# Kernel tuning notes

Measured on AMD Instinct MI355X. Metric: run time of the kernel, lower is better.

Reference implementation:

```python
import jax, jax.numpy as jnp
import numpy as np

M = 2048                      # image side (self.M)
INPUT_SHAPE = (362, 362)      # default forward arg; only used for pad sizing
N_ANGLES = 32
THETA = np.linspace(0.0, np.pi, N_ANGLES)  # radians, as the source uses np.cos(angle)


def _dct_mat(N):
    # DCT-II with norm='ortho': C[k, n] = s_k * cos(pi*(n+0.5)*k/N)
    n = np.arange(N)
    C = np.cos(np.pi * (n[None, :] + 0.5) * n[:, None] / N)
    scale = np.full((N, 1), np.sqrt(2.0 / N))
    scale[0, 0] = np.sqrt(1.0 / N)
    return jnp.asarray((C * scale).astype(np.float32))


def _pad_width():
    diagonal = np.sqrt(2) * max(INPUT_SHAPE)
    pad = [int(np.ceil(diagonal - s)) for s in INPUT_SHAPE]
    new_center = [(s + p) // 2 for s, p in zip(INPUT_SHAPE, pad)]
    old_center = [s // 2 for s in INPUT_SHAPE]
    pad_before = [nc - oc for oc, nc in zip(old_center, new_center)]
    return [(pb, p - pb) for pb, p in zip(pad_before, pad)]


def setup_inputs() -> dict:
    key = jax.random.key(0)
    image = jax.random.normal(key, (M, M), dtype=jnp.float32)
    return {"image": image}


def _forward(image):
    # --- 2D DCT-II (ortho), separable: D = C @ x @ C^T ---
    C = _dct_mat(M)
    d = C @ image @ C.T

    # --- pad (widths derived from input_shape as in the source) ---
    padded = jnp.pad(d, _pad_width())          # [P, P], P = 2198
    P = padded.shape[0]
    center = P // 2

    xs = jnp.arange(P, dtype=jnp.float32)
    yy, xx = jnp.meshgrid(xs, xs, indexing='ij')   # output row (y) / col (x) grid
    angles = jnp.asarray(THETA, dtype=jnp.float32)

    def one_angle(carry, ang):
        cos_a = jnp.cos(ang)
        sin_a = jnp.sin(ang)
        # ImageProjectiveTransformV3 maps output (x, y) -> input coords
        x_in = cos_a * xx + sin_a * yy - center * (cos_a + sin_a - 1.0)
        y_in = -sin_a * xx + cos_a * yy - center * (cos_a - sin_a - 1.0)
        x0 = jnp.floor(x_in)
        y0 = jnp.floor(y_in)
        wx = x_in - x0
        wy = y_in - y0
        # fill_mode='WRAP': wrap sample coordinates modulo image size
        x0i = jnp.mod(x0.astype(jnp.int32), P)
        x1i = (x0i + 1) % P
        y0i = jnp.mod(y0.astype(jnp.int32), P)
        y1i = (y0i + 1) % P
        v00 = padded[y0i, x0i]
        v01 = padded[y0i, x1i]
        v10 = padded[y1i, x0i]
        v11 = padded[y1i, x1i]
        rotated = (1.0 - wy) * ((1.0 - wx) * v00 + wx * v01) \
                + wy * ((1.0 - wx) * v10 + wx * v11)
        # radon line: reduce over rows (axis=0)
        return carry, rotated.sum(axis=0)

    _, lines = jax.lax.scan(one_angle, 0, angles)   # [A, P]
    y = lines.T                                     # [P, A] == tf.transpose(A)
    return y / jnp.max(y)


def reference(image):
    return _forward(image)
```

## Files before the change

kernel.cpp:

```cpp
#include <hip/hip_runtime.h>
#include <hip/hip_bf16.h>
#include <math.h>

#define PDIM 2198
#define PDIM2 2252
#define PADB 75
#define NANG 32
#define NLINE (NANG * PDIM)

#define CB 32
#define RW 32
#define NWIN 69
#define TS 48
#define TSTRIDE 52
#define NBUF 4

typedef __attribute__((ext_vector_type(8))) short bf16x8;
typedef __attribute__((ext_vector_type(4))) float f32x4;

#define GLOAD_LDS16(g, l)                                              \
    __builtin_amdgcn_global_load_lds(                                  \
        (const __attribute__((address_space(1))) void*)(g),            \
        (__attribute__((address_space(3))) void*)(l), 16, 0, 0)

#if __has_builtin(__builtin_amdgcn_fractf)
#define FRACTF(x) __builtin_amdgcn_fractf(x)
#else
#define FRACTF(x) ((x) - floorf(x))
#endif

__global__ void gen_dct(__hip_bfloat16* __restrict__ C) {
    int idx = blockIdx.x * 256 + threadIdx.x;
    int k = idx >> 11;
    int n = idx & 2047;
    int t = ((2 * n + 1) * k) & 8191;
    float s = sqrtf(((k == 0) ? 1.0f : 2.0f) / 2048.0f);
    C[idx] = __float2bfloat16(s * cospif((float)t * (1.0f / 4096.0f)));
}

__global__ void cvt_img(const float* __restrict__ in, __hip_bfloat16* __restrict__ out) {
    int i = (blockIdx.x * 256 + threadIdx.x) * 4;
    float4 v = *(const float4*)(in + i);
    out[i + 0] = __float2bfloat16(v.x);
    out[i + 1] = __float2bfloat16(v.y);
    out[i + 2] = __float2bfloat16(v.z);
    out[i + 3] = __float2bfloat16(v.w);
}

template<int F32OUT>
__global__ __launch_bounds__(256) void gemm_bt(const __hip_bfloat16* __restrict__ A,
                                               const __hip_bfloat16* __restrict__ B,
                                               void* __restrict__ out,
                                               int ldo, int off) {
    __shared__ __hip_bfloat16 Al[128 * 32];
    __shared__ __hip_bfloat16 Bl[64 * 32];
    const int tid = threadIdx.x;
    const int wid = tid >> 6;
    const int lane = tid & 63;
    const int wr = wid >> 1, wc = wid & 1;
    const int l15 = lane & 15, lhi = lane >> 4;
    const int row0 = blockIdx.y * 128;
    const int col0 = blockIdx.x * 64;

    const __hip_bfloat16* gA = A + (size_t)(row0 + wid * 32 + (lane >> 2)) * 2048 + (lane & 3) * 8;
    const __hip_bfloat16* gB = B + (size_t)(col0 + wid * 16 + (lane >> 2)) * 2048 + (lane & 3) * 8;
    __hip_bfloat16* lA = Al + wid * 1024;
    __hip_bfloat16* lB = Bl + wid * 512;

    f32x4 acc[4][2] = {};

    for (int k0 = 0; k0 < 2048; k0 += 32) {
        GLOAD_LDS16(gA + k0, lA);
        GLOAD_LDS16(gA + 16 * 2048 + k0, lA + 16 * 32);
        GLOAD_LDS16(gB + k0, lB);
        __syncthreads();
        bf16x8 af[4], bfr[2];
#pragma unroll
        for (int m = 0; m < 4; ++m)
            af[m] = *(const bf16x8*)(Al + (wr * 64 + m * 16 + l15) * 32 + lhi * 8);
#pragma unroll
        for (int n = 0; n < 2; ++n)
            bfr[n] = *(const bf16x8*)(Bl + (wc * 32 + n * 16 + l15) * 32 + lhi * 8);
#pragma unroll
        for (int m = 0; m < 4; ++m)
#pragma unroll
            for (int n = 0; n < 2; ++n)
                acc[m][n] = __builtin_amdgcn_mfma_f32_16x16x32_bf16(af[m], bfr[n],
                                                                    acc[m][n], 0, 0, 0);
        __syncthreads();
    }

#pragma unroll
    for (int m = 0; m < 4; ++m) {
        const int row = row0 + wr * 64 + m * 16 + lhi * 4;
#pragma unroll
        for (int n = 0; n < 2; ++n) {
            const int col = col0 + wc * 32 + n * 16 + l15;
            f32x4 v = acc[m][n];
            if (F32OUT) {
                float* p = (float*)out + (size_t)(col + off) * ldo + off + row;
                p[0] = v[0]; p[1] = v[1]; p[2] = v[2]; p[3] = v[3];
            } else {
                __hip_bfloat16* p = (__hip_bfloat16*)out + (size_t)col * 2048 + row;
                p[0] = __float2bfloat16(v[0]);
                p[1] = __float2bfloat16(v[1]);
                p[2] = __float2bfloat16(v[2]);
                p[3] = __float2bfloat16(v[3]);
            }
        }
    }
}

struct AngleArgs {
    float ca[NANG], sa[NANG], ox[NANG], oy[NANG];
};

__global__ __launch_bounds__(256) void radon6(const float* __restrict__ padded,
                                              float* __restrict__ lines,
                                              AngleArgs args) {
    __shared__ float tile[NBUF][TS * TSTRIDE];
    __shared__ float red[4][8];
    const int a = blockIdx.y;
    const int c0 = blockIdx.x * CB;
    const int t = threadIdx.x;
    const int wid = t >> 6, lane = t & 63;
    const int cl = lane >> 3;
    const int rl = lane & 7;
    const int c = c0 + wid * 8 + cl;
    const float ca = args.ca[a], sa = args.sa[a];
    const float ox = args.ox[a], oy = args.oy[a];

    const float cf = (float)c;
    const float xbase = fmaf(ca, cf, ox);
    const float ybase = fmaf(-sa, cf, oy);

    const float xbMin = fminf(fmaf(ca, (float)c0, ox), fmaf(ca, (float)(c0 + CB - 1), ox));
    const float ybMin = fminf(fmaf(-sa, (float)c0, oy), fmaf(-sa, (float)(c0 + CB - 1), oy));
    const bool caPos = (ca >= 0.0f);

    float sum = 0.0f;

    auto origin = [&](int w, int& bx0, int& by0) {
        const float rx = (float)(w * RW);
        const float ry = caPos ? rx : (float)(w * RW + RW - 1);
        bx0 = (int)floorf(fmaf(sa, rx, xbMin)) - 1;
        by0 = (int)floorf(fmaf(ca, ry, ybMin)) - 1;
    };

    auto stage = [&](int buf, int bx0, int by0) {
        int bxs = bx0;
        bxs += (bxs < 0) ? PDIM : 0;
        bxs -= (bxs >= PDIM) ? PDIM : 0;
        const int slab = wid * 12;
#pragma unroll
        for (int iss = 0; iss < 3; ++iss) {
            const int d = iss * 256 + lane * 4;
            if (d < 12 * TSTRIDE) {
                const int rr = d / TSTRIDE;
                const int col = d - rr * TSTRIDE;
                int gy = by0 + slab + rr;
                gy += (gy < 0) ? PDIM : 0;
                gy -= (gy >= PDIM) ? PDIM : 0;
                GLOAD_LDS16(padded + (size_t)gy * PDIM2 + bxs + col,
                            &tile[buf][slab * TSTRIDE + iss * 256]);
            }
        }
    };

    auto compute = [&](int r0, int buf, int bx0, int by0, bool last) {
        const float xbb = xbase - (float)bx0;
        const float ybb = ybase - (float)by0;
        const float* tb = &tile[buf][0];
#pragma unroll
        for (int k = 0; k < 4; ++k) {
            const int r = r0 + rl + 8 * k;
            const float rf = (float)r;
            const float xl = fmaf(sa, rf, xbb);
            const float yl = fmaf(ca, rf, ybb);
            const int xi = (int)xl;
            const int yi = (int)yl;
            const float wx = FRACTF(xl);
            const float wy = FRACTF(yl);
            const float* p = tb + yi * TSTRIDE + xi;
            const float v00 = p[0], v01 = p[1];
            const float v10 = p[TSTRIDE], v11 = p[TSTRIDE + 1];
            const float top = fmaf(wx, v01 - v00, v00);
            const float bot = fmaf(wx, v11 - v10, v10);
            if (!last || r < PDIM) sum = fmaf(wy, bot - top, sum + top);
        }
    };

    int bx[NWIN > 0 ? 4 : 4], by[4];
    origin(0, bx[0], by[0]);
    stage(0, bx[0], by[0]);
    origin(1, bx[1], by[1]);
    stage(1, bx[1], by[1]);
    for (int w = 0; w < NWIN; ++w) {
        if (w + 2 < NWIN) {
            int bxn, byn;
            origin(w + 2, bxn, byn);
            bx[(w + 2) & 3] = bxn; by[(w + 2) & 3] = byn;
            stage((w + 2) & 3, bxn, byn);
        }
        if (w < NWIN - 2)       asm volatile("s_waitcnt vmcnt(6)" ::: "memory");
        else if (w == NWIN - 2) asm volatile("s_waitcnt vmcnt(3)" ::: "memory");
        else                    asm volatile("s_waitcnt vmcnt(0)" ::: "memory");
        __builtin_amdgcn_s_barrier();
        __builtin_amdgcn_sched_barrier(0);
        compute(w * RW, w & 3, bx[w & 3], by[w & 3], w == NWIN - 1);
    }

    sum += __shfl_xor(sum, 1, 64);
    sum += __shfl_xor(sum, 2, 64);
    sum += __shfl_xor(sum, 4, 64);
    if (rl == 0) red[wid][cl] = sum;
    __syncthreads();
    if (t < 32 && c0 + t < PDIM)
        lines[a * PDIM + c0 + t] = red[t >> 3][t & 7];
}

__global__ __launch_bounds__(256) void max_k(const float* __restrict__ lines,
                                             unsigned int* __restrict__ gmax) {
    const int idx = blockIdx.x * 256 + threadIdx.x;
    float m = (idx < NLINE) ? lines[idx] : -3.4e38f;
#pragma unroll
    for (int off = 32; off > 0; off >>= 1)
        m = fmaxf(m, __shfl_down(m, off, 64));
    __shared__ float wm[4];
    const int lane = threadIdx.x & 63, wid = threadIdx.x >> 6;
    if (lane == 0) wm[wid] = m;
    __syncthreads();
    if (threadIdx.x == 0) {
        float bm = fmaxf(fmaxf(wm[0], wm[1]), fmaxf(wm[2], wm[3]));
        unsigned int b = __float_as_uint(bm);
        unsigned int key = (b & 0x80000000u) ? ~b : (b | 0x80000000u);
        atomicMax(gmax, key);
    }
}

__global__ void norm_k(const float* __restrict__ lines,
                       const unsigned int* __restrict__ gmax,
                       float* __restrict__ out) {
    int idx = blockIdx.x * 256 + threadIdx.x;
    if (idx >= NLINE) return;
    unsigned int u = *gmax;
    unsigned int b = (u & 0x80000000u) ? (u & 0x7fffffffu) : ~u;
    float mx = __uint_as_float(b);
    int c = idx >> 5;
    int a = idx & 31;
    out[idx] = lines[(size_t)a * PDIM + c] / mx;
}

extern "C" void kernel_launch(void* const* d_in, const int* in_sizes, int n_in,
                              void* d_out, int out_size, void* d_ws, size_t ws_size,
                              hipStream_t stream) {
    (void)in_sizes; (void)n_in; (void)out_size; (void)ws_size;
    const float* img = (const float*)d_in[0];
    float* out = (float*)d_out;

    __hip_bfloat16* Cbf   = (__hip_bfloat16*)d_ws;
    __hip_bfloat16* imgbf = Cbf + 4194304;
    __hip_bfloat16* uT    = imgbf + 4194304;
    float* padded  = (float*)(uT + 4194304);
    float* lines   = padded + (size_t)PDIM * PDIM2;
    unsigned int* gmax = (unsigned int*)(lines + NLINE);

    hipMemsetAsync(padded, 0, (size_t)PDIM * PDIM2 * sizeof(float), stream);
    hipMemsetAsync(gmax, 0, sizeof(unsigned int), stream);

    gen_dct<<<16384, 256, 0, stream>>>(Cbf);
    cvt_img<<<4096, 256, 0, stream>>>(img, imgbf);

    gemm_bt<0><<<dim3(32, 16), 256, 0, stream>>>(imgbf, Cbf, uT, 2048, 0);
    gemm_bt<1><<<dim3(32, 16), 256, 0, stream>>>(uT, Cbf, padded, PDIM2, PADB);

    AngleArgs aa;
    for (int i = 0; i < NANG; ++i) {
        float th = (float)((double)i * 3.14159265358979323846 / 31.0);
        float ca = (float)cos((double)th);
        float sa = (float)sin((double)th);
        aa.ca[i] = ca;
        aa.sa[i] = sa;
        aa.ox[i] = -1099.0f * (ca + sa - 1.0f);
        aa.oy[i] = -1099.0f * (ca - sa - 1.0f);
    }
    radon6<<<dim3(NWIN, NANG), 256, 0, stream>>>(padded, lines, aa);
    max_k<<<(NLINE + 255) / 256, 256, 0, stream>>>(lines, gmax);
    norm_k<<<(NLINE + 255) / 256, 256, 0, stream>>>(lines, gmax, out);
}
```

Measured before the change: 318.8 us.

## Zero only pad borders and use triple-buffered radon staging

Replaces the full memset of the padded buffer with a kernel that zeroes only the pad border rows and columns, since the GEMM writes the interior. This avoids rewriting roughly 20 MB of memory. The radon kernel moves from four LDS buffers to three, issues each prefetch after the barrier, and specializes the last-window bounds check at compile time. Fewer buffers cut LDS use and could raise occupancy, but the prefetch is now issued later, which may expose more load latency.

```diff
diff --git a/kernel.cpp b/kernel.cpp
--- a/kernel.cpp
+++ b/kernel.cpp
@@ -13,10 +13,12 @@
 #define NWIN 69
 #define TS 48
 #define TSTRIDE 52
-#define NBUF 4
+#define NBUF 3
 
 typedef __attribute__((ext_vector_type(8))) short bf16x8;
 typedef __attribute__((ext_vector_type(4))) float f32x4;
+
+template<bool L> struct BoolC { static constexpr bool value = L; };
 
 #define GLOAD_LDS16(g, l)                                              \
     __builtin_amdgcn_global_load_lds(                                  \
@@ -45,6 +47,24 @@
     out[i + 1] = __float2bfloat16(v.y);
     out[i + 2] = __float2bfloat16(v.z);
     out[i + 3] = __float2bfloat16(v.w);
+}
+
+__global__ __launch_bounds__(256) void pad_zero(float* __restrict__ padded) {
+    int idx = blockIdx.x * 256 + threadIdx.x;
+    const int TOPBOT = 2 * PADB * PDIM2;
+    if (idx < TOPBOT) {
+        int r = idx / PDIM2;
+        int c = idx - r * PDIM2;
+        int row = (r < PADB) ? r : (2048 + r);
+        padded[(size_t)row * PDIM2 + c] = 0.0f;
+    } else {
+        int i2 = idx - TOPBOT;
+        if (i2 >= 2048 * 204) return;
+        int rr = i2 / 204;
+        int s = i2 - rr * 204;
+        int col = (s < PADB) ? s : (2048 + s);
+        padded[(size_t)(PADB + rr) * PDIM2 + col] = 0.0f;
+    }
 }
 
 template<int F32OUT>
@@ -115,7 +135,7 @@
     float ca[NANG], sa[NANG], ox[NANG], oy[NANG];
 };
 
-__global__ __launch_bounds__(256) void radon6(const float* __restrict__ padded,
+__global__ __launch_bounds__(256) void radon7(const float* __restrict__ padded,
                                               float* __restrict__ lines,
                                               AngleArgs args) {
     __shared__ float tile[NBUF][TS * TSTRIDE];
@@ -167,7 +187,7 @@
         }
     };
 
-    auto compute = [&](int r0, int buf, int bx0, int by0, bool last) {
+    auto computeT = [&](int r0, int buf, int bx0, int by0, auto lastc) {
         const float xbb = xbase - (float)bx0;
         const float ybb = ybase - (float)by0;
         const float* tb = &tile[buf][0];
@@ -186,28 +206,28 @@
             const float v10 = p[TSTRIDE], v11 = p[TSTRIDE + 1];
             const float top = fmaf(wx, v01 - v00, v00);
             const float bot = fmaf(wx, v11 - v10, v10);
-            if (!last || r < PDIM) sum = fmaf(wy, bot - top, sum + top);
+            if (!decltype(lastc)::value || r < PDIM) sum = fmaf(wy, bot - top, sum + top);
         }
     };
 
-    int bx[NWIN > 0 ? 4 : 4], by[4];
-    origin(0, bx[0], by[0]);
-    stage(0, bx[0], by[0]);
-    origin(1, bx[1], by[1]);
-    stage(1, bx[1], by[1]);
+    int bxr[3], byr[3];
+    origin(0, bxr[0], byr[0]);
+    stage(0, bxr[0], byr[0]);
+    origin(1, bxr[1], byr[1]);
+    stage(1, bxr[1], byr[1]);
     for (int w = 0; w < NWIN; ++w) {
-        if (w + 2 < NWIN) {
-            int bxn, byn;
-            origin(w + 2, bxn, byn);
-            bx[(w + 2) & 3] = bxn; by[(w + 2) & 3] = byn;
-            stage((w + 2) & 3, bxn, byn);
-        }
-        if (w < NWIN - 2)       asm volatile("s_waitcnt vmcnt(6)" ::: "memory");
-        else if (w == NWIN - 2) asm volatile("s_waitcnt vmcnt(3)" ::: "memory");
-        else                    asm volatile("s_waitcnt vmcnt(0)" ::: "memory");
+        if (w < NWIN - 1) asm volatile("s_waitcnt vmcnt(3)" ::: "memory");
+        else              asm volatile("s_waitcnt vmcnt(0)" ::: "memory");
         __builtin_amdgcn_s_barrier();
         __builtin_amdgcn_sched_barrier(0);
-        compute(w * RW, w & 3, bx[w & 3], by[w & 3], w == NWIN - 1);
+        if (w + 2 < NWIN) {
+            const int wn = (w + 2) % 3;
+            origin(w + 2, bxr[wn], byr[wn]);
+            stage(wn, bxr[wn], byr[wn]);
+        }
+        const int wi = w % 3;
+        if (w < NWIN - 1) computeT(w * RW, wi, bxr[wi], byr[wi], BoolC<false>{});
+        else              computeT(w * RW, wi, bxr[wi], byr[wi], BoolC<true>{});
     }
 
     sum += __shfl_xor(sum, 1, 64);
@@ -265,11 +285,11 @@
     float* lines   = padded + (size_t)PDIM * PDIM2;
     unsigned int* gmax = (unsigned int*)(lines + NLINE);
 
-    hipMemsetAsync(padded, 0, (size_t)PDIM * PDIM2 * sizeof(float), stream);
-    hipMemsetAsync(gmax, 0, sizeof(unsigned int), stream);
+    (void)hipMemsetAsync(gmax, 0, sizeof(unsigned int), stream);
 
     gen_dct<<<16384, 256, 0, stream>>>(Cbf);
     cvt_img<<<4096, 256, 0, stream>>>(img, imgbf);
+    pad_zero<<<(2 * PADB * PDIM2 + 2048 * 204 + 255) / 256, 256, 0, stream>>>(padded);
 
     gemm_bt<0><<<dim3(32, 16), 256, 0, stream>>>(imgbf, Cbf, uT, 2048, 0);
     gemm_bt<1><<<dim3(32, 16), 256, 0, stream>>>(uT, Cbf, padded, PDIM2, PADB);
@@ -284,7 +304,7 @@
         aa.ox[i] = -1099.0f * (ca + sa - 1.0f);
         aa.oy[i] = -1099.0f * (ca - sa - 1.0f);
     }
-    radon6<<<dim3(NWIN, NANG), 256, 0, stream>>>(padded, lines, aa);
+    radon7<<<dim3(NWIN, NANG), 256, 0, stream>>>(padded, lines, aa);
     max_k<<<(NLINE + 255) / 256, 256, 0, stream>>>(lines, gmax);
     norm_k<<<(NLINE + 255) / 256, 256, 0, stream>>>(lines, gmax, out);
 }
```

Measured after the change: 304.6 us. 4.5% less time.
